# Kernel optimization log

Measured on AMD Instinct MI355X. Metric: run time of the kernel, lower is better.

## Reference

```python
import jax, jax.numpy as jnp
import numpy as np

N, E, B, F_IN, C, K = 200000, 3200000, 128, 128, 10, 30
D_CAT = 97  # 32+32+32+1 concatenated GCN outputs


def setup_inputs() -> dict:
    key = jax.random.key(0)
    ks = jax.random.split(key, 12)
    s = 0.1
    return {
        "x": jax.random.normal(ks[0], (N, F_IN), jnp.float32),
        "edge_index": jax.random.randint(ks[1], (2, E), 0, N, jnp.int32),
        "batch": jnp.sort(jax.random.randint(ks[2], (N,), 0, B, jnp.int32)),
        "W1": jax.random.normal(ks[3], (F_IN, 32), jnp.float32) * s,
        "b1": jnp.zeros((32,), jnp.float32),
        "W2": jax.random.normal(ks[4], (32, 32), jnp.float32) * s,
        "b2": jnp.zeros((32,), jnp.float32),
        "W3": jax.random.normal(ks[5], (32, 32), jnp.float32) * s,
        "b3": jnp.zeros((32,), jnp.float32),
        "W4": jax.random.normal(ks[6], (32, 1), jnp.float32) * s,
        "b4": jnp.zeros((1,), jnp.float32),
        "conv5_w": jax.random.normal(ks[7], (16, 1, 97), jnp.float32) * s,
        "conv5_b": jnp.zeros((16,), jnp.float32),
        "conv6_w": jax.random.normal(ks[8], (32, 16, 5), jnp.float32) * s,
        "conv6_b": jnp.zeros((32,), jnp.float32),
        "fc1_w": jax.random.normal(ks[9], (352, 128), jnp.float32) * s,
        "fc1_b": jnp.zeros((128,), jnp.float32),
        "fc2_w": jax.random.normal(ks[10], (128, C), jnp.float32) * s,
        "fc2_b": jnp.zeros((C,), jnp.float32),
    }


def _gcn(x, W, b, src, dst, enorm, self_norm):
    # PyG GCNConv: h = xW; out = sum_j norm_ij * h_j (incl. self loop) + b
    h = x @ W
    agg = jax.ops.segment_sum(h[src] * enorm[:, None], dst, num_segments=h.shape[0])
    return agg + h * self_norm[:, None] + b


def _conv1d(x, w, b, stride):
    y = jax.lax.conv_general_dilated(x, w, (stride,), 'VALID',
                                     dimension_numbers=('NCH', 'OIH', 'NCH'))
    return y + b[None, :, None]


def reference(x, edge_index, batch, W1, b1, W2, b2, W3, b3, W4, b4,
              conv5_w, conv5_b, conv6_w, conv6_b, fc1_w, fc1_b, fc2_w, fc2_b):
    src, dst = edge_index[0], edge_index[1]
    # remove_self_loops (zero edge weight) then GCN adds self loop of weight 1
    w = (src != dst).astype(x.dtype)
    deg = jax.ops.segment_sum(w, dst, num_segments=N) + 1.0
    dinv = jax.lax.rsqrt(deg)
    enorm = w * dinv[src] * dinv[dst]   # per-edge sym norm
    self_norm = 1.0 / deg               # self-loop norm = dinv[i]^2

    x1 = jnp.tanh(_gcn(x, W1, b1, src, dst, enorm, self_norm))
    x2 = jnp.tanh(_gcn(x1, W2, b2, src, dst, enorm, self_norm))
    x3 = jnp.tanh(_gcn(x2, W3, b3, src, dst, enorm, self_norm))
    x4 = jnp.tanh(_gcn(x3, W4, b4, src, dst, enorm, self_norm))
    xc = jnp.concatenate([x1, x2, x3, x4], axis=-1)  # [N, 97]

    # SortAggregation(k=30): per-graph top-k nodes by last channel (descending)
    keyf = xc[:, -1]
    graph_ids = jnp.arange(B, dtype=batch.dtype)
    scores = jnp.where(batch[None, :] == graph_ids[:, None], keyf[None, :],
                       jnp.float32(-jnp.inf))         # [B, N]
    topv, topi = jax.lax.top_k(scores, K)              # [B, K]
    feats = xc[topi]                                   # [B, K, 97]
    feats = jnp.where(jnp.isfinite(topv)[..., None], feats, 0.0)  # pad rows -> 0
    z = feats.reshape(B, 1, K * D_CAT)                 # [B, 1, 2910]

    z = jax.nn.relu(_conv1d(z, conv5_w, conv5_b, 97))  # [B, 16, 30]
    z = jax.lax.reduce_window(z, -jnp.inf, jax.lax.max,
                              (1, 1, 2), (1, 1, 2), 'VALID')  # [B, 16, 15]
    z = jax.nn.relu(_conv1d(z, conv6_w, conv6_b, 1))   # [B, 32, 11]
    z = z.reshape(B, -1)                               # [B, 352]
    h = jax.nn.relu(z @ fc1_w + fc1_b)                 # dropout = identity (eval)
    return jax.nn.log_softmax(h @ fc2_w + fc2_b, axis=-1)
```

## Files before the change

kernel.cpp:

```cpp
#include <hip/hip_runtime.h>
#include <math.h>

#define TPB 256
#define TOPK 30
#define NGRAPH 128
#define TKCAP 4096
#define BSHIFT 11
#define NBMAX 128
#define FSHIFT 8
#define FCAP 4608


__global__ void bhist(const int* __restrict__ src, const int* __restrict__ dst,
                      int* __restrict__ btot, int E) {
    __shared__ int bcnt[NBMAX];
    int t = threadIdx.x;
    int base = blockIdx.x * 2048;
    int lim = E - base; if (lim > 2048) lim = 2048;
    for (int i = t; i < NBMAX; i += 256) bcnt[i] = 0;
    __syncthreads();
    for (int i = t; i < lim; i += 256) {
        int s = src[base + i], d = dst[base + i];
        if (s != d) atomicAdd(&bcnt[d >> BSHIFT], 1);
    }
    __syncthreads();
    for (int i = t; i < NBMAX; i += 256)
        if (bcnt[i] > 0) atomicAdd(&btot[i], bcnt[i]);
}

__global__ void bucket_scan(const int* __restrict__ btot, int* __restrict__ bbase,
                            int nbuckets) {
    __shared__ int ls[NBMAX];
    int t = threadIdx.x;
    int v = (t < nbuckets) ? btot[t] : 0;
    ls[t] = v;
    __syncthreads();
    for (int o = 1; o < NBMAX; o <<= 1) {
        int x = 0;
        if (t >= o) x = ls[t - o];
        __syncthreads();
        ls[t] += x;
        __syncthreads();
    }
    if (t < nbuckets) bbase[t] = ls[t] - v;
}

__global__ void bin_edges(const int* __restrict__ src, const int* __restrict__ dst,
                          const int* __restrict__ bbase_g, int* __restrict__ gcur,
                          int2* __restrict__ scratch, int E) {
    __shared__ int2 eds[2048];
    __shared__ int bcnt[NBMAX], bbase[NBMAX], boff[NBMAX];
    int t = threadIdx.x;
    int base = blockIdx.x * 2048;
    int lim = E - base; if (lim > 2048) lim = 2048;
    for (int i = t; i < NBMAX; i += 256) { bcnt[i] = 0; boff[i] = 0; }
    __syncthreads();
    for (int i = t; i < lim; i += 256) {
        int s = src[base + i], d = dst[base + i];
        if (s == d) d = -1;
        eds[i] = make_int2(s, d);
        if (d >= 0) atomicAdd(&bcnt[d >> BSHIFT], 1);
    }
    __syncthreads();
    for (int i = t; i < NBMAX; i += 256) {
        if (bcnt[i] > 0)
            bbase[i] = bbase_g[i] + atomicAdd(&gcur[i], bcnt[i]);
    }
    __syncthreads();
    for (int i = t; i < lim; i += 256) {
        int2 ed = eds[i];
        if (ed.y >= 0) {
            int b = ed.y >> BSHIFT;
            int pos = bbase[b] + atomicAdd(&boff[b], 1);
            scratch[pos] = ed;
        }
    }
}

__global__ void bucket_count(const int2* __restrict__ scratch,
                             const int* __restrict__ bbase, const int* __restrict__ btot,
                             int* __restrict__ rowptr, float* __restrict__ dinv,
                             float* __restrict__ snorm, int N, int NB) {
    __shared__ int hist[1 << BSHIFT];
    __shared__ int ls2[256];
    int b = blockIdx.x, t = threadIdx.x;
    int nlo = b << BSHIFT;
    int nn = N - nlo; if (nn > (1 << BSHIFT)) nn = 1 << BSHIFT;
    for (int i = t; i < (1 << BSHIFT); i += 256) hist[i] = 0;
    __syncthreads();
    int lo = bbase[b], hi = lo + btot[b];
    for (int e = lo + t; e < hi; e += 256)
        atomicAdd(&hist[scratch[e].y - nlo], 1);
    __syncthreads();
    int loc[8]; int run = 0;
    #pragma unroll
    for (int j = 0; j < 8; ++j) { loc[j] = run; run += hist[t * 8 + j]; }
    ls2[t] = run;
    __syncthreads();
    for (int o = 1; o < 256; o <<= 1) {
        int x = (t >= o) ? ls2[t - o] : 0;
        __syncthreads();
        ls2[t] += x;
        __syncthreads();
    }
    int base = bbase[b] + ls2[t] - run;
    #pragma unroll
    for (int j = 0; j < 8; ++j) {
        int i = t * 8 + j;
        if (i < nn) {
            rowptr[nlo + i] = base + loc[j];
            int c = hist[i];
            float deg = (float)c + 1.0f;
            dinv[nlo + i] = 1.0f / sqrtf(deg);
            snorm[nlo + i] = 1.0f / deg;
        }
    }
    if (b == NB - 1 && t == 0) rowptr[N] = bbase[b] + btot[b];
}

__global__ __launch_bounds__(256) void scatter_sort(const int2* __restrict__ scratch,
                                                    const int* __restrict__ bbase,
                                                    const int* __restrict__ btot,
                                                    const int* __restrict__ rowptr,
                                                    const float* __restrict__ dinv,
                                                    int2* __restrict__ eprec, int N) {
    __shared__ int srcA[FCAP], dstA[FCAP], inv[FCAP];
    __shared__ int hist[1 << FSHIFT];
    __shared__ int hcur[1 << FSHIFT];
    __shared__ int kcnt;
    int f = blockIdx.x, t = threadIdx.x;
    int nlo = f << FSHIFT;
    int nhi = nlo + (1 << FSHIFT); if (nhi > N) nhi = N;
    int lo = rowptr[nlo], hi = rowptr[nhi];
    int span = hi - lo;
    int cb = f >> (BSHIFT - FSHIFT);
    int clo = bbase[cb], chi = clo + btot[cb];
    for (int i = t; i < (1 << FSHIFT); i += 256) hist[i] = 0;
    if (t == 0) kcnt = 0;
    __syncthreads();
    if (span <= FCAP) {
        for (int e = clo + t; e < chi; e += 256) {
            int2 ed = scratch[e];
            if ((ed.y >> FSHIFT) == f) {
                int p = atomicAdd(&kcnt, 1);
                srcA[p] = ed.x; dstA[p] = ed.y;
                atomicAdd(&hist[ed.y - nlo], 1);
            }
        }
        __syncthreads();
        int v = hist[t];
        hcur[t] = v;
        __syncthreads();
        for (int o = 1; o < 256; o <<= 1) {
            int x = (t >= o) ? hcur[t - o] : 0;
            __syncthreads();
            hcur[t] += x;
            __syncthreads();
        }
        int excl = hcur[t] - v;
        __syncthreads();
        hcur[t] = excl;
        __syncthreads();
        for (int i = t; i < span; i += 256) {
            int slot = atomicAdd(&hcur[dstA[i] - nlo], 1);
            inv[slot] = i;
        }
        __syncthreads();
        for (int p = t; p < span; p += 256) {
            int i = inv[p];
            int s = srcA[i], d = dstA[i];
            eprec[lo + p] = make_int2(s, __float_as_int(dinv[s] * dinv[d]));
        }
    } else {
        for (int e = clo + t; e < chi; e += 256) {
            int2 ed = scratch[e];
            if ((ed.y >> FSHIFT) == f) {
                int d = ed.y;
                int p = rowptr[d] + atomicAdd(&hist[d - nlo], 1);
                eprec[p] = make_int2(ed.x, __float_as_int(dinv[ed.x] * dinv[d]));
            }
        }
    }
}


__global__ void mm_128_32(const float* __restrict__ X, const float* __restrict__ W,
                          float* __restrict__ H, int n) {
    __shared__ float Ws[128 * 32];
    __shared__ float xs[32 * 128];
    int t = threadIdx.x;
    int rbase = blockIdx.x * 32;
    #pragma unroll
    for (int j = 0; j < 4; ++j) {
        int idx = t + 256 * j;
        *(float4*)(Ws + idx * 4) = *(const float4*)(W + idx * 4);
        int row = rbase + (idx >> 5);
        float4 v = make_float4(0.f, 0.f, 0.f, 0.f);
        if (row < n) v = *(const float4*)(X + (long)rbase * 128 + idx * 4);
        *(float4*)(xs + idx * 4) = v;
    }
    __syncthreads();
    int c4 = (t & 7) * 4, r = t >> 3;
    int row = rbase + r;
    if (row >= n) return;
    float ac0 = 0.f, ac1 = 0.f, ac2 = 0.f, ac3 = 0.f;
    #pragma unroll 8
    for (int k0 = 0; k0 < 128; k0 += 4) {
        float4 xv = *(const float4*)(xs + r * 128 + k0);
        #pragma unroll
        for (int j = 0; j < 4; ++j) {
            float xj = (j == 0) ? xv.x : (j == 1) ? xv.y : (j == 2) ? xv.z : xv.w;
            float4 wv = *(const float4*)(Ws + (k0 + j) * 32 + c4);
            ac0 += xj * wv.x; ac1 += xj * wv.y; ac2 += xj * wv.z; ac3 += xj * wv.w;
        }
    }
    *(float4*)(H + (long)row * 32 + c4) = make_float4(ac0, ac1, ac2, ac3);
}

__global__ void mm_32_32(const float* __restrict__ X, const float* __restrict__ W,
                         float* __restrict__ H, int n) {
    __shared__ float Ws[32 * 32];
    __shared__ float xs[32 * 32];
    int t = threadIdx.x;
    int rbase = blockIdx.x * 32;
    {
        *(float4*)(Ws + t * 4) = *(const float4*)(W + t * 4);
        int row = rbase + (t >> 3);
        float4 v = make_float4(0.f, 0.f, 0.f, 0.f);
        if (row < n) v = *(const float4*)(X + (long)rbase * 32 + t * 4);
        *(float4*)(xs + t * 4) = v;
    }
    __syncthreads();
    int c4 = (t & 7) * 4, r = t >> 3;
    int row = rbase + r;
    if (row >= n) return;
    float ac0 = 0.f, ac1 = 0.f, ac2 = 0.f, ac3 = 0.f;
    #pragma unroll
    for (int k0 = 0; k0 < 32; k0 += 4) {
        float4 xv = *(const float4*)(xs + r * 32 + k0);
        #pragma unroll
        for (int j = 0; j < 4; ++j) {
            float xj = (j == 0) ? xv.x : (j == 1) ? xv.y : (j == 2) ? xv.z : xv.w;
            float4 wv = *(const float4*)(Ws + (k0 + j) * 32 + c4);
            ac0 += xj * wv.x; ac1 += xj * wv.y; ac2 += xj * wv.z; ac3 += xj * wv.w;
        }
    }
    *(float4*)(H + (long)row * 32 + c4) = make_float4(ac0, ac1, ac2, ac3);
}

__global__ void mm_32_1(const float* __restrict__ X, const float* __restrict__ W,
                        float* __restrict__ H4, int n) {
    int gid = blockIdx.x * blockDim.x + threadIdx.x;
    int node = gid >> 3, l = gid & 7;
    if (node >= n) return;
    float4 v = *(const float4*)(X + (long)node * 32 + l * 4);
    float s = v.x * W[l * 4] + v.y * W[l * 4 + 1] + v.z * W[l * 4 + 2] + v.w * W[l * 4 + 3];
    s += __shfl_xor(s, 1, 64);
    s += __shfl_xor(s, 2, 64);
    s += __shfl_xor(s, 4, 64);
    if (l == 0) H4[node] = s;
}


__global__ void agg32(const float* __restrict__ H, const int2* __restrict__ eprec,
                      const int* __restrict__ rowptr,
                      const float* __restrict__ snorm, const float* __restrict__ bias,
                      float* __restrict__ OUT, int n) {
    int gid = blockIdx.x * blockDim.x + threadIdx.x;
    int node = gid >> 3, l = gid & 7;
    if (node >= n) return;
    int beg = rowptr[node], end = rowptr[node + 1];
    float ax = 0.f, ay = 0.f, az = 0.f, aw = 0.f;
    int e0 = beg;
    for (; e0 + 8 <= end; e0 += 8) {
        int2 ed = eprec[e0 + l];
        int ss[8]; float ww[8];
        #pragma unroll
        for (int j = 0; j < 8; ++j) {
            ss[j] = __shfl(ed.x, j, 8);
            ww[j] = __shfl(__int_as_float(ed.y), j, 8);
        }
        float4 hv[8];
        #pragma unroll
        for (int j = 0; j < 8; ++j)
            hv[j] = *(const float4*)(H + (long)ss[j] * 32 + l * 4);
        #pragma unroll
        for (int j = 0; j < 8; ++j) {
            ax += hv[j].x * ww[j]; ay += hv[j].y * ww[j];
            az += hv[j].z * ww[j]; aw += hv[j].w * ww[j];
        }
    }
    if (e0 < end) {
        int m = end - e0;
        int2 ed = (l < m) ? eprec[e0 + l] : make_int2(0, 0);
        for (int j = 0; j < m; ++j) {
            int s = __shfl(ed.x, j, 8);
            float w = __shfl(__int_as_float(ed.y), j, 8);
            float4 hv = *(const float4*)(H + (long)s * 32 + l * 4);
            ax += hv.x * w; ay += hv.y * w; az += hv.z * w; aw += hv.w * w;
        }
    }
    float sn = snorm[node];
    float4 hv = *(const float4*)(H + (long)node * 32 + l * 4);
    float4 bv = *(const float4*)(bias + l * 4);
    float4 o;
    o.x = tanhf(ax + hv.x * sn + bv.x);
    o.y = tanhf(ay + hv.y * sn + bv.y);
    o.z = tanhf(az + hv.z * sn + bv.z);
    o.w = tanhf(aw + hv.w * sn + bv.w);
    *(float4*)(OUT + (long)node * 32 + l * 4) = o;
}

__global__ void agg1(const float* __restrict__ H4, const int2* __restrict__ eprec,
                     const int* __restrict__ rowptr,
                     const float* __restrict__ snorm, const float* __restrict__ b4,
                     float* __restrict__ X4, int n) {
    int node = blockIdx.x * blockDim.x + threadIdx.x;
    if (node >= n) return;
    int beg = rowptr[node], end = rowptr[node + 1];
    float acc = 0.f;
    for (int e = beg; e < end; ++e) {
        int2 ed = eprec[e];
        acc += H4[ed.x] * __int_as_float(ed.y);
    }
    X4[node] = tanhf(acc + H4[node] * snorm[node] + b4[0]);
}


__global__ __launch_bounds__(256) void topk_head(
        const float* __restrict__ x1, const float* __restrict__ x2,
        const float* __restrict__ x3, const float* __restrict__ x4,
        const int* __restrict__ batch, int Nn,
        const float* __restrict__ w5, const float* __restrict__ b5,
        const float* __restrict__ w6, const float* __restrict__ b6,
        const float* __restrict__ fw1, const float* __restrict__ fb1,
        const float* __restrict__ fw2, const float* __restrict__ fb2,
        float* __restrict__ out) {
    int g = blockIdx.x;
    int t = threadIdx.x;
    __shared__ int topi_l[TOPK];
    __shared__ int selg[TOPK];
    __shared__ int begend[2];
    __shared__ float vals[TKCAP];
    __shared__ float wbv[4];
    __shared__ int wbi[4];
    __shared__ float feats[TOPK][97];
    __shared__ float c5[16][30];
    __shared__ float p6[16][15];
    __shared__ float z[352];
    __shared__ float hh[128];
    __shared__ float oo[10];

    if (t == 0) {
        int lo = 0, hi = Nn;
        while (lo < hi) { int m = (lo + hi) >> 1; if (batch[m] < g) lo = m + 1; else hi = m; }
        begend[0] = lo;
        lo = 0; hi = Nn;
        while (lo < hi) { int m = (lo + hi) >> 1; if (batch[m] < g + 1) lo = m + 1; else hi = m; }
        begend[1] = lo;
    }
    __syncthreads();
    int beg = begend[0], end = begend[1];
    int range = end - beg;

    if (range <= 2048) {
        if (t < 64) {
            float rv[32];
            #pragma unroll
            for (int j = 0; j < 32; ++j) {
                int i = t + (j << 6);
                rv[j] = (i < range) ? x4[beg + i] : -INFINITY;
            }
            for (int k = 0; k < TOPK; ++k) {
                float best = -INFINITY;
                int bj = -1;
                #pragma unroll
                for (int j = 0; j < 32; ++j)
                    if (rv[j] > best) { best = rv[j]; bj = j; }
                int bi = (bj < 0) ? 0x7fffffff : (bj << 6) + t;
                #pragma unroll
                for (int off = 1; off < 64; off <<= 1) {
                    float ov = __shfl_xor(best, off, 64);
                    int oi = __shfl_xor(bi, off, 64);
                    if (ov > best || (ov == best && oi < bi)) { best = ov; bi = oi; }
                }
                if (t == 0)
                    topi_l[k] = (bi == 0x7fffffff) ? -1 : beg + bi;
                if (bi != 0x7fffffff && (bi & 63) == t) {
                    int wj = bi >> 6;
                    #pragma unroll
                    for (int j = 0; j < 32; ++j)
                        if (j == wj) rv[j] = -INFINITY;
                }
            }
        }
    } else {
        int lim = range < TKCAP ? range : TKCAP;
        for (int i = t; i < lim; i += 256) vals[i] = x4[beg + i];
        __syncthreads();
        for (int k = 0; k < TOPK; ++k) {
            float best = -INFINITY;
            int bi = 0x7fffffff;
            for (int i = t; i < lim; i += 256) {
                float v = vals[i];
                if (v > best) { best = v; bi = i; }
            }
            for (int i = TKCAP + t; i < range; i += 256) {
                int gi = beg + i;
                bool taken = false;
                for (int j = 0; j < k; ++j)
                    if (selg[j] == gi) { taken = true; break; }
                if (taken) continue;
                float v = vals[0];
                v = x4[gi];
                if (v > best || (v == best && i < bi)) { best = v; bi = i; }
            }
            #pragma unroll
            for (int off = 1; off < 64; off <<= 1) {
                float ov = __shfl_xor(best, off, 64);
                int oi = __shfl_xor(bi, off, 64);
                if (ov > best || (ov == best && oi < bi)) { best = ov; bi = oi; }
            }
            if ((t & 63) == 0) { wbv[t >> 6] = best; wbi[t >> 6] = bi; }
            __syncthreads();
            if (t == 0) {
                float bv = wbv[0]; int bi0 = wbi[0];
                for (int wv = 1; wv < 4; ++wv)
                    if (wbv[wv] > bv || (wbv[wv] == bv && wbi[wv] < bi0)) { bv = wbv[wv]; bi0 = wbi[wv]; }
                int gl = (bi0 == 0x7fffffff) ? -1 : beg + bi0;
                selg[k] = gl;
                topi_l[k] = gl;
                if (bi0 != 0x7fffffff && bi0 < TKCAP) vals[bi0] = -INFINITY;
            }
            __syncthreads();
        }
    }
    __syncthreads();

    for (int idx = t; idx < TOPK * 97; idx += 256) {
        int k = idx / 97, j = idx % 97;
        int node = topi_l[k];
        float v = 0.f;
        if (node >= 0) {
            if (j < 32) v = x1[(long)node * 32 + j];
            else if (j < 64) v = x2[(long)node * 32 + (j - 32)];
            else if (j < 96) v = x3[(long)node * 32 + (j - 64)];
            else v = x4[node];
        }
        feats[k][j] = v;
    }
    __syncthreads();

    for (int idx = t; idx < 16 * 30; idx += 256) {
        int oc = idx / 30, k = idx % 30;
        float acc = b5[oc];
        for (int j = 0; j < 97; ++j) acc += w5[oc * 97 + j] * feats[k][j];
        c5[oc][k] = fmaxf(acc, 0.f);
    }
    __syncthreads();

    for (int idx = t; idx < 16 * 15; idx += 256) {
        int oc = idx / 15, k = idx % 15;
        p6[oc][k] = fmaxf(c5[oc][2 * k], c5[oc][2 * k + 1]);
    }
    __syncthreads();

    for (int idx = t; idx < 32 * 11; idx += 256) {
        int oc = idx / 11, tt = idx % 11;
        float acc = b6[oc];
        for (int ic = 0; ic < 16; ++ic)
            for (int j = 0; j < 5; ++j)
                acc += w6[(oc * 16 + ic) * 5 + j] * p6[ic][tt + j];
        z[idx] = fmaxf(acc, 0.f);
    }
    __syncthreads();

    if (t < 128) {
        float acc = fb1[t];
        for (int i = 0; i < 352; ++i) acc += z[i] * fw1[i * 128 + t];
        hh[t] = fmaxf(acc, 0.f);
    }
    __syncthreads();

    if (t < 10) {
        float acc = fb2[t];
        for (int j = 0; j < 128; ++j) acc += hh[j] * fw2[j * 10 + t];
        oo[t] = acc;
    }
    __syncthreads();

    if (t < 10) {
        float m = -INFINITY;
        for (int c = 0; c < 10; ++c) m = fmaxf(m, oo[c]);
        float s = 0.f;
        for (int c = 0; c < 10; ++c) s += expf(oo[c] - m);
        out[g * 10 + t] = oo[t] - m - logf(s);
    }
}


extern "C" void kernel_launch(void* const* d_in, const int* in_sizes, int n_in,
                              void* d_out, int out_size, void* d_ws, size_t ws_size,
                              hipStream_t stream) {
    const float* x     = (const float*)d_in[0];
    const int*   ei    = (const int*)d_in[1];
    const int*   batch = (const int*)d_in[2];
    const float* W1 = (const float*)d_in[3];
    const float* b1 = (const float*)d_in[4];
    const float* W2 = (const float*)d_in[5];
    const float* b2 = (const float*)d_in[6];
    const float* W3 = (const float*)d_in[7];
    const float* b3 = (const float*)d_in[8];
    const float* W4 = (const float*)d_in[9];
    const float* b4 = (const float*)d_in[10];
    const float* w5 = (const float*)d_in[11];
    const float* b5 = (const float*)d_in[12];
    const float* w6 = (const float*)d_in[13];
    const float* b6 = (const float*)d_in[14];
    const float* fw1 = (const float*)d_in[15];
    const float* fb1 = (const float*)d_in[16];
    const float* fw2 = (const float*)d_in[17];
    const float* fb2 = (const float*)d_in[18];

    const int N = in_sizes[0] / 128;
    const int E = in_sizes[1] / 2;
    const int* src = ei;
    const int* dst = ei + E;

    char* w = (char*)d_ws;
    size_t off = 0;
    auto alloc = [&](size_t bytes) -> void* {
        void* p = w + off;
        off = (off + bytes + 255) & ~(size_t)255;
        return p;
    };

    int*   gcur   = (int*)alloc(NBMAX * 4);
    int*   btot   = (int*)alloc(NBMAX * 4);
    int*   bbase  = (int*)alloc(NBMAX * 4);
    int*   rowptr = (int*)alloc((size_t)(N + 1) * 4);
    float* dinv   = (float*)alloc((size_t)N * 4);
    float* snorm  = (float*)alloc((size_t)N * 4);
    int2*  eprec  = (int2*)alloc((size_t)E * 8);
    float* hbuf   = (float*)alloc((size_t)N * 32 * 4);
    float* x1     = (float*)alloc((size_t)N * 32 * 4);
    float* x2     = (float*)alloc((size_t)N * 32 * 4);
    float* x3     = (float*)alloc((size_t)N * 32 * 4);
    float* h4     = (float*)alloc((size_t)N * 4);
    float* x4     = (float*)alloc((size_t)N * 4);

    int2* scratch = (int2*)hbuf;

    hipMemsetAsync(gcur, 0, 2 * NBMAX * 4, stream);

    const int NB = (N + (1 << BSHIFT) - 1) >> BSHIFT;
    const int NF = (N + (1 << FSHIFT) - 1) >> FSHIFT;
    const int EB = (E + 2047) / 2048;

    bhist<<<EB, TPB, 0, stream>>>(src, dst, btot, E);
    bucket_scan<<<1, NBMAX, 0, stream>>>(btot, bbase, NB);
    bin_edges<<<EB, TPB, 0, stream>>>(src, dst, bbase, gcur, scratch, E);
    bucket_count<<<NB, TPB, 0, stream>>>(scratch, bbase, btot, rowptr, dinv, snorm, N, NB);
    scatter_sort<<<NF, 256, 0, stream>>>(scratch, bbase, btot, rowptr, dinv, eprec, N);

    mm_128_32<<<(N + 31) / 32, 256, 0, stream>>>(x, W1, hbuf, N);
    agg32<<<((size_t)N * 8 + TPB - 1) / TPB, TPB, 0, stream>>>(hbuf, eprec, rowptr,
                                                               snorm, b1, x1, N);
    mm_32_32<<<(N + 31) / 32, 256, 0, stream>>>(x1, W2, hbuf, N);
    agg32<<<((size_t)N * 8 + TPB - 1) / TPB, TPB, 0, stream>>>(hbuf, eprec, rowptr,
                                                               snorm, b2, x2, N);
    mm_32_32<<<(N + 31) / 32, 256, 0, stream>>>(x2, W3, hbuf, N);
    agg32<<<((size_t)N * 8 + TPB - 1) / TPB, TPB, 0, stream>>>(hbuf, eprec, rowptr,
                                                               snorm, b3, x3, N);
    mm_32_1<<<((size_t)N * 8 + TPB - 1) / TPB, TPB, 0, stream>>>(x3, W4, h4, N);
    agg1<<<(N + TPB - 1) / TPB, TPB, 0, stream>>>(h4, eprec, rowptr, snorm, b4, x4, N);

    topk_head<<<NGRAPH, 256, 0, stream>>>(x1, x2, x3, x4, batch, N,
                                          w5, b5, w6, b6, fw1, fb1, fw2, fb2,
                                          (float*)d_out);
}
```

Baseline: 638.8 us.

## Add second-level binning pass so scatter_sort reads only its own edges

Adds a bin2 kernel that redistributes coarse-bucketed edges into fine 256-node bins using rowptr offsets and per-bin atomic cursors. scatter_sort then reads a contiguous span of its own edges instead of each of eight blocks scanning the whole coarse bucket and filtering. This removes roughly eightfold redundant reads of the scratch buffer, at the cost of an extra kernel launch and one extra read/write pass over all edges. It also drops a dead load in the top-k fallback path.

Measured after the change: 565.2 us. -11.5%, faster.

```diff
diff --git a/kernel.cpp b/kernel.cpp
--- a/kernel.cpp
+++ b/kernel.cpp
@@ -8,6 +8,7 @@
 #define BSHIFT 11
 #define NBMAX 128
 #define FSHIFT 8
+#define NFMAX 800
 #define FCAP 4608
 
 
@@ -118,34 +119,53 @@
     if (b == NB - 1 && t == 0) rowptr[N] = bbase[b] + btot[b];
 }
 
-__global__ __launch_bounds__(256) void scatter_sort(const int2* __restrict__ scratch,
-                                                    const int* __restrict__ bbase,
-                                                    const int* __restrict__ btot,
+__global__ void bin2(const int2* __restrict__ scratch, const int* __restrict__ rowptr,
+                     int* __restrict__ fcur, int2* __restrict__ scratch2, int N, int E) {
+    __shared__ int fcnt[NFMAX], fbase[NFMAX], foff[NFMAX];
+    int t = threadIdx.x;
+    int En = rowptr[N];
+    int base = blockIdx.x * 8192;
+    if (base >= En) return;
+    int lim = En - base; if (lim > 8192) lim = 8192;
+    for (int i = t; i < NFMAX; i += 256) { fcnt[i] = 0; foff[i] = 0; }
+    __syncthreads();
+    for (int i = t; i < lim; i += 256) {
+        int d = scratch[base + i].y;
+        atomicAdd(&fcnt[d >> FSHIFT], 1);
+    }
+    __syncthreads();
+    for (int fi = t; fi < NFMAX; fi += 256) {
+        if (fcnt[fi] > 0)
+            fbase[fi] = rowptr[fi << FSHIFT] + atomicAdd(&fcur[fi], fcnt[fi]);
+    }
+    __syncthreads();
+    for (int i = t; i < lim; i += 256) {
+        int2 ed = scratch[base + i];
+        int fi = ed.y >> FSHIFT;
+        int pos = fbase[fi] + atomicAdd(&foff[fi], 1);
+        scratch2[pos] = ed;
+    }
+}
+
+__global__ __launch_bounds__(256) void scatter_sort(const int2* __restrict__ scratch2,
                                                     const int* __restrict__ rowptr,
                                                     const float* __restrict__ dinv,
                                                     int2* __restrict__ eprec, int N) {
     __shared__ int srcA[FCAP], dstA[FCAP], inv[FCAP];
     __shared__ int hist[1 << FSHIFT];
     __shared__ int hcur[1 << FSHIFT];
-    __shared__ int kcnt;
     int f = blockIdx.x, t = threadIdx.x;
     int nlo = f << FSHIFT;
     int nhi = nlo + (1 << FSHIFT); if (nhi > N) nhi = N;
     int lo = rowptr[nlo], hi = rowptr[nhi];
     int span = hi - lo;
-    int cb = f >> (BSHIFT - FSHIFT);
-    int clo = bbase[cb], chi = clo + btot[cb];
     for (int i = t; i < (1 << FSHIFT); i += 256) hist[i] = 0;
-    if (t == 0) kcnt = 0;
     __syncthreads();
     if (span <= FCAP) {
-        for (int e = clo + t; e < chi; e += 256) {
-            int2 ed = scratch[e];
-            if ((ed.y >> FSHIFT) == f) {
-                int p = atomicAdd(&kcnt, 1);
-                srcA[p] = ed.x; dstA[p] = ed.y;
-                atomicAdd(&hist[ed.y - nlo], 1);
-            }
+        for (int i = t; i < span; i += 256) {
+            int2 ed = scratch2[lo + i];
+            srcA[i] = ed.x; dstA[i] = ed.y;
+            atomicAdd(&hist[ed.y - nlo], 1);
         }
         __syncthreads();
         int v = hist[t];
@@ -172,13 +192,11 @@
             eprec[lo + p] = make_int2(s, __float_as_int(dinv[s] * dinv[d]));
         }
     } else {
-        for (int e = clo + t; e < chi; e += 256) {
-            int2 ed = scratch[e];
-            if ((ed.y >> FSHIFT) == f) {
-                int d = ed.y;
-                int p = rowptr[d] + atomicAdd(&hist[d - nlo], 1);
-                eprec[p] = make_int2(ed.x, __float_as_int(dinv[ed.x] * dinv[d]));
-            }
+        for (int e = lo + t; e < hi; e += 256) {
+            int2 ed = scratch2[e];
+            int d = ed.y;
+            int p = rowptr[d] + atomicAdd(&hist[d - nlo], 1);
+            eprec[p] = make_int2(ed.x, __float_as_int(dinv[ed.x] * dinv[d]));
         }
     }
 }
@@ -411,8 +429,7 @@
                 for (int j = 0; j < k; ++j)
                     if (selg[j] == gi) { taken = true; break; }
                 if (taken) continue;
-                float v = vals[0];
-                v = x4[gi];
+                float v = x4[gi];
                 if (v > best || (v == best && i < bi)) { best = v; bi = i; }
             }
             #pragma unroll
@@ -537,6 +554,7 @@
 
     int*   gcur   = (int*)alloc(NBMAX * 4);
     int*   btot   = (int*)alloc(NBMAX * 4);
+    int*   fcur   = (int*)alloc(NFMAX * 4);
     int*   bbase  = (int*)alloc(NBMAX * 4);
     int*   rowptr = (int*)alloc((size_t)(N + 1) * 4);
     float* dinv   = (float*)alloc((size_t)N * 4);
@@ -549,9 +567,10 @@
     float* h4     = (float*)alloc((size_t)N * 4);
     float* x4     = (float*)alloc((size_t)N * 4);
 
-    int2* scratch = (int2*)hbuf;
-
-    hipMemsetAsync(gcur, 0, 2 * NBMAX * 4, stream);
+    int2* scratch  = (int2*)hbuf;
+    int2* scratch2 = (int2*)x1;
+
+    hipMemsetAsync(gcur, 0, (size_t)(2 * NBMAX + NFMAX) * 4, stream);
 
     const int NB = (N + (1 << BSHIFT) - 1) >> BSHIFT;
     const int NF = (N + (1 << FSHIFT) - 1) >> FSHIFT;
@@ -561,7 +580,8 @@
     bucket_scan<<<1, NBMAX, 0, stream>>>(btot, bbase, NB);
     bin_edges<<<EB, TPB, 0, stream>>>(src, dst, bbase, gcur, scratch, E);
     bucket_count<<<NB, TPB, 0, stream>>>(scratch, bbase, btot, rowptr, dinv, snorm, N, NB);
-    scatter_sort<<<NF, 256, 0, stream>>>(scratch, bbase, btot, rowptr, dinv, eprec, N);
+    bin2<<<(E + 8191) / 8192, TPB, 0, stream>>>(scratch, rowptr, fcur, scratch2, N, E);
+    scatter_sort<<<NF, 256, 0, stream>>>(scratch2, rowptr, dinv, eprec, N);
 
     mm_128_32<<<(N + 31) / 32, 256, 0, stream>>>(x, W1, hbuf, N);
     agg32<<<((size_t)N * 8 + TPB - 1) / TPB, TPB, 0, stream>>>(hbuf, eprec, rowptr,
```
